# Optimization experiments

Hardware: AMD Instinct MI355X
Metric: run time of the kernel (lower is better)

## Reference

```python
import jax, jax.numpy as jnp
import numpy as np

NUM_HEADS = 32
HEAD_DIM = 64
ROPE_THETA = 10000.0


def _rope_cos_sin(position_ids, head_dim, theta):
    # inv_freq: [head_dim/2]
    half = head_dim // 2
    inv_freq = 1.0 / (theta ** (jnp.arange(0, half, dtype=jnp.float32) * 2.0 / head_dim))
    angles = position_ids.astype(jnp.float32)[..., None] * inv_freq  # [B,S,half]
    return jnp.cos(angles), jnp.sin(angles)


def _apply_rope(x, cos, sin):
    # x: [B,S,H,hd]; cos/sin: [B,S,half] -> broadcast over heads (rotate-half, Llama style)
    half = x.shape[-1] // 2
    x1, x2 = x[..., :half], x[..., half:]
    c = cos[:, :, None, :]
    s = sin[:, :, None, :]
    return jnp.concatenate([x1 * c - x2 * s, x2 * c + x1 * s], axis=-1)


def setup_inputs() -> dict:
    key = jax.random.key(0)
    ks = jax.random.split(key, 8)
    B, S, D = 2, 2048, 2048
    hidden_states = jax.random.normal(ks[0], (B, S, D), dtype=jnp.float32)
    # causal additive mask (is_causal=False in IpexSDP; mask carries causality)
    causal = jnp.tril(jnp.ones((S, S), dtype=jnp.bool_))
    attention_mask = jnp.where(causal, 0.0, -1e9).astype(jnp.float32)[None, None, :, :]
    attention_mask = jnp.broadcast_to(attention_mask, (B, 1, S, S))
    position_ids = jnp.broadcast_to(jnp.arange(S, dtype=jnp.int64)[None, :], (B, S))
    scale = 0.02
    qkv_w = jax.random.normal(ks[1], (3, D, D), dtype=jnp.float32) * scale
    qkv_b = jax.random.normal(ks[2], (3, D), dtype=jnp.float32) * scale
    o_w = jax.random.normal(ks[3], (D, D), dtype=jnp.float32) * scale
    o_b = jax.random.normal(ks[4], (D,), dtype=jnp.float32) * scale
    residual = jax.random.normal(ks[5], (B, S, D), dtype=jnp.float32)
    return {
        'hidden_states': hidden_states,
        'attention_mask': attention_mask,
        'position_ids': position_ids,
        'qkv_w': qkv_w,
        'qkv_b': qkv_b,
        'o_w': o_w,
        'o_b': o_b,
        'residual': residual,
    }


def reference(hidden_states, attention_mask, position_ids, qkv_w, qkv_b, o_w, o_b, residual):
    B, S, D = hidden_states.shape
    H, hd = NUM_HEADS, HEAD_DIM
    # fused QKV projection (weights stored transposed: x @ W), matching mm_qkv_out
    qkv = jnp.einsum('bsd,tde->tbse', hidden_states, qkv_w) + qkv_b[:, None, None, :]
    q = qkv[0].reshape(B, S, H, hd)
    k = qkv[1].reshape(B, S, H, hd)
    v = qkv[2].reshape(B, S, H, hd)
    cos, sin = _rope_cos_sin(position_ids, hd, ROPE_THETA)
    q = _apply_rope(q, cos, sin)
    k = _apply_rope(k, cos, sin)
    scale = 1.0 / jnp.sqrt(jnp.asarray(hd, dtype=hidden_states.dtype))
    # [B,H,S,S]
    scores = jnp.einsum('bqhd,bkhd->bhqk', q, k) * scale + attention_mask
    probs = jax.nn.softmax(scores, axis=-1)
    attn = jnp.einsum('bhqk,bkhd->bqhd', probs, v).reshape(B, S, D)
    # o-proj fused with bias + residual add (matmul_add_add)
    out = attn @ o_w + o_b + residual
    return out
```

## Files before the change

kernel.cpp:

```cpp
#include <hip/hip_runtime.h>
#include <stdint.h>
#include <stdio.h>

#define D_MODEL 2048
#define SEQ     2048
#define NHEADS  32
#define HDIM    64
#define BATCH   2
#define BH      (BATCH * NHEADS)
#define GK      2048

typedef unsigned short u16;
typedef unsigned int   u32;
typedef __attribute__((ext_vector_type(8))) short short8;
typedef __attribute__((ext_vector_type(4))) short s16x4;
typedef __attribute__((ext_vector_type(4))) float f32x4;
typedef __attribute__((ext_vector_type(4))) u32   u32x4;
typedef __attribute__((ext_vector_type(2))) u32   u32x2;

__device__ __forceinline__ float bf2f(u16 x) {
  union { u32 u; float f; } c; c.u = ((u32)x) << 16; return c.f;
}
__device__ __forceinline__ u16 f2bf(float f) {
  union { float f; u32 u; } c; c.f = f;
  u32 u = c.u;
  return (u16)((u + 0x7FFFu + ((u >> 16) & 1u)) >> 16);
}
__device__ __forceinline__ u32 fbits(float f) {
  union { float f; u32 u; } c; c.f = f; return c.u;
}

typedef const __attribute__((address_space(1))) u32* gas_t;
typedef __attribute__((address_space(3))) u32* las_t;
__device__ __forceinline__ void gll16(const void* g, void* l) {
  __builtin_amdgcn_global_load_lds((gas_t)g, (las_t)l, 16, 0, 0);
}

__device__ __forceinline__ void swiz_mn(int pid, int nx, int& mtile, int& ntile) {
  int chunk = 8 * nx;
  int grp = pid / chunk, loc = pid - grp * chunk;
  mtile = grp * 8 + (loc & 7);
  ntile = loc >> 3;
}

__global__ __launch_bounds__(256) void cvt_k(const float* __restrict__ in,
                                             u16* __restrict__ out) {
  int id = blockIdx.x * 256 + threadIdx.x;
  f32x4 v = *(const f32x4*)&in[(size_t)id * 4];
  alignas(8) u16 o[4];
#pragma unroll
  for (int j = 0; j < 4; j++) o[j] = f2bf(v[j]);
  *(u32x2*)&out[(size_t)id * 4] = *(const u32x2*)o;
}

__global__ __launch_bounds__(256) void transpose_cvt_k(const float* __restrict__ qkv_w,
                                                       const float* __restrict__ o_w,
                                                       u16* __restrict__ outT) {
  __shared__ u16 tile[64][72];
  const int z = blockIdx.z;
  const float* inz = (z < 3) ? qkv_w + (size_t)z * D_MODEL * D_MODEL : o_w;
  u16* outz = outT + (size_t)z * D_MODEL * D_MODEL;
  const int r0 = blockIdx.y * 64, c0 = blockIdx.x * 64;
  const int t = threadIdx.x;
  const int lrow = t >> 4, lcol4 = (t & 15) * 4;
#pragma unroll
  for (int i = 0; i < 4; i++) {
    int r = lrow + i * 16;
    f32x4 v = *(const f32x4*)&inz[(size_t)(r0 + r) * D_MODEL + (c0 + lcol4)];
#pragma unroll
    for (int j = 0; j < 4; j++) tile[r][lcol4 + j] = f2bf(v[j]);
  }
  __syncthreads();
  const int row = t >> 3, col8 = (t & 7) * 8;
#pragma unroll
  for (int i = 0; i < 2; i++) {
    int r = row + i * 32;
    alignas(16) u16 vals[8];
#pragma unroll
    for (int j = 0; j < 8; j++) vals[j] = tile[col8 + j][r];
    *(u32x4*)&outz[(size_t)(c0 + r) * D_MODEL + (r0 + col8)] = *(const u32x4*)vals;
  }
}

__device__ __forceinline__ void gemm128(const u16* __restrict__ A, const u16* __restrict__ BT,
                                        int m0, int n0, u16* As, u16* Bs, f32x4 acc[4][4]) {
  const int t = threadIdx.x;
  const int lane = t & 63, w = t >> 6;
  const int quad = lane >> 4, l16 = lane & 15;
  const int wr = w >> 1, wc = w & 1;
  const int ldr = lane >> 2, ldc = (lane & 3) * 8;
#pragma unroll
  for (int mt = 0; mt < 4; mt++)
#pragma unroll
    for (int nt = 0; nt < 4; nt++)
#pragma unroll
      for (int i = 0; i < 4; i++) acc[mt][nt][i] = 0.0f;

  for (int k0 = 0; k0 < GK; k0 += 32) {
    __syncthreads();
#pragma unroll
    for (int i = 0; i < 2; i++) {
      int rbase = w * 32 + i * 16;
      gll16(&A[(size_t)(m0 + rbase + ldr) * GK + k0 + ldc], &As[rbase * 32]);
      gll16(&BT[(size_t)(n0 + rbase + ldr) * GK + k0 + ldc], &Bs[rbase * 32]);
    }
    __syncthreads();
    short8 af[4], bf[4];
#pragma unroll
    for (int mt = 0; mt < 4; mt++)
      af[mt] = *(const short8*)&As[(wr * 64 + mt * 16 + l16) * 32 + quad * 8];
#pragma unroll
    for (int nt = 0; nt < 4; nt++)
      bf[nt] = *(const short8*)&Bs[(wc * 64 + nt * 16 + l16) * 32 + quad * 8];
#pragma unroll
    for (int mt = 0; mt < 4; mt++)
#pragma unroll
      for (int nt = 0; nt < 4; nt++)
        acc[mt][nt] = __builtin_amdgcn_mfma_f32_16x16x32_bf16(af[mt], bf[nt], acc[mt][nt], 0, 0, 0);
  }
}

__global__ __launch_bounds__(256) void qkv_gemm_k(const u16* __restrict__ A, const u16* __restrict__ BT,
                                                  const float* __restrict__ bias,
                                                  u16* __restrict__ Qb, u16* __restrict__ Kb,
                                                  u16* __restrict__ Vbt) {
  __shared__ u16 As[128 * 32], Bs[128 * 32];
  f32x4 acc[4][4];
  int mtile, ntile;
  swiz_mn(blockIdx.x, 48, mtile, ntile);
  const int m0 = mtile * 128, n0 = ntile * 128;
  gemm128(A, BT, m0, n0, As, Bs, acc);
  const int t = threadIdx.x, lane = t & 63, quad = lane >> 4, l16 = lane & 15;
  const int w = t >> 6, wr = w >> 1, wc = w & 1;
  const int tsel = n0 >> 11;

  if (tsel < 2) {
    u16* dst = tsel ? Kb : Qb;
#pragma unroll
    for (int p = 0; p < 2; p++) {
      int nlo = n0 + wc * 64 + p * 16 + l16;
      float blo = bias[nlo], bhi = bias[nlo + 32];
      int j = p * 16 + l16;
      float inv = __expf((float)j * -0.28782313662425572f);
      int h = (nlo & 2047) >> 6;
#pragma unroll
      for (int mt = 0; mt < 4; mt++) {
#pragma unroll
        for (int r = 0; r < 4; r++) {
          int m = m0 + wr * 64 + mt * 16 + quad * 4 + r;
          int b = m >> 11, s = m & (SEQ - 1);
          float sn, cs;
          __sincosf((float)s * inv, &sn, &cs);
          float x1 = acc[mt][p][r] + blo;
          float x2 = acc[mt][p + 2][r] + bhi;
          size_t base = ((size_t)((b * NHEADS + h) * SEQ + s)) * HDIM;
          dst[base + j]      = f2bf(x1 * cs - x2 * sn);
          dst[base + j + 32] = f2bf(x2 * cs + x1 * sn);
        }
      }
    }
  } else {
#pragma unroll
    for (int nt = 0; nt < 4; nt++) {
      int n = n0 + wc * 64 + nt * 16 + l16;
      float bv = bias[n];
      int e = n & 2047, h = e >> 6, d = e & 63;
#pragma unroll
      for (int mt = 0; mt < 4; mt++) {
        int m0r = m0 + wr * 64 + mt * 16 + quad * 4;
        int b = m0r >> 11, s0 = m0r & (SEQ - 1);
        alignas(8) u16 o4[4];
#pragma unroll
        for (int r = 0; r < 4; r++) o4[r] = f2bf(acc[mt][nt][r] + bv);
        *(u32x2*)&Vbt[((size_t)((b * NHEADS + h) * HDIM + d)) * SEQ + s0] = *(const u32x2*)o4;
      }
    }
  }
}

__global__ __launch_bounds__(256) void oproj_gemm_k(const u16* __restrict__ A, const u16* __restrict__ BT,
                                                    const float* __restrict__ bias,
                                                    const float* __restrict__ resid,
                                                    float* __restrict__ out) {
  __shared__ u16 As[128 * 32], Bs[128 * 32];
  f32x4 acc[4][4];
  int mtile, ntile;
  swiz_mn(blockIdx.x, 16, mtile, ntile);
  const int m0 = mtile * 128, n0 = ntile * 128;
  gemm128(A, BT, m0, n0, As, Bs, acc);
  const int t = threadIdx.x, lane = t & 63, quad = lane >> 4, l16 = lane & 15;
  const int w = t >> 6, wr = w >> 1, wc = w & 1;
#pragma unroll
  for (int nt = 0; nt < 4; nt++) {
    int n = n0 + wc * 64 + nt * 16 + l16;
    float bv = bias[n];
#pragma unroll
    for (int mt = 0; mt < 4; mt++) {
#pragma unroll
      for (int r = 0; r < 4; r++) {
        int m = m0 + wr * 64 + mt * 16 + quad * 4 + r;
        size_t oi = (size_t)m * D_MODEL + n;
        out[oi] = acc[mt][nt][r] + bv + resid[oi];
      }
    }
  }
}

__global__ __launch_bounds__(256, 4) void attn_k(const u16* __restrict__ Qb,
                                                 const u16* __restrict__ Kb,
                                                 const u16* __restrict__ Vbt,
                                                 u16* __restrict__ attn) {
  __shared__ u16 smem[128 * 72];
  u16* Ks = smem;
  u16* Vt = smem + 64 * 72;
  const int blk = blockIdx.x;
  const int qt16 = blk & 15, bh = blk >> 4;
  const int b = bh >> 5, h = bh & 31;
  const int t = threadIdx.x, w = t >> 6, lane = t & 63, quad = lane >> 4, l16 = lane & 15;
  const int qbase = qt16 * 128, qw = qbase + w * 32;
  const size_t bho = (size_t)bh * SEQ * HDIM;
  const size_t vbo = (size_t)bh * HDIM * SEQ;

  short8 qf[2][2];
#pragma unroll
  for (int qt = 0; qt < 2; qt++)
#pragma unroll
    for (int kd = 0; kd < 2; kd++) {
      short8 v = *(const short8*)&Qb[bho + (size_t)(qw + qt * 16 + l16) * HDIM + kd * 32 + quad * 8];
#pragma unroll
      for (int i = 0; i < 8; i++) {
        float f = bf2f((u16)v[i]) * 0.125f;
        v[i] = (short)f2bf(f);
      }
      qf[qt][kd] = v;
    }

  f32x4 Oacc[4][2];
  float mrow[2] = {-1e30f, -1e30f}, lrow[2] = {0.0f, 0.0f};
#pragma unroll
  for (int dt = 0; dt < 4; dt++)
#pragma unroll
    for (int qt = 0; qt < 2; qt++)
#pragma unroll
      for (int i = 0; i < 4; i++) Oacc[dt][qt][i] = 0.0f;

  const int srow = t >> 3, scol = (t & 7) * 8;
  const int kend = qbase + 128;

  for (int key0 = 0; key0 < kend; key0 += 64) {
    __syncthreads();
    *(u32x4*)&Ks[srow * 72 + scol] =
        *(const u32x4*)&Kb[bho + (size_t)(key0 + srow) * HDIM + scol];
    *(u32x4*)&Ks[(srow + 32) * 72 + scol] =
        *(const u32x4*)&Kb[bho + (size_t)(key0 + srow + 32) * HDIM + scol];
    *(u32x4*)&Vt[srow * 72 + scol] =
        *(const u32x4*)&Vbt[vbo + (size_t)srow * SEQ + key0 + scol];
    *(u32x4*)&Vt[(srow + 32) * 72 + scol] =
        *(const u32x4*)&Vbt[vbo + (size_t)(srow + 32) * SEQ + key0 + scol];
    __syncthreads();

    if (key0 <= qw + 31) {
      f32x4 sacc[4][2];
#pragma unroll
      for (int kt = 0; kt < 4; kt++) {
        short8 kf0 = *(const short8*)&Ks[(kt * 16 + l16) * 72 + quad * 8];
        short8 kf1 = *(const short8*)&Ks[(kt * 16 + l16) * 72 + 32 + quad * 8];
#pragma unroll
        for (int qt = 0; qt < 2; qt++) {
#pragma unroll
          for (int i = 0; i < 4; i++) sacc[kt][qt][i] = 0.0f;
          sacc[kt][qt] = __builtin_amdgcn_mfma_f32_16x16x32_bf16(kf0, qf[qt][0], sacc[kt][qt], 0, 0, 0);
          sacc[kt][qt] = __builtin_amdgcn_mfma_f32_16x16x32_bf16(kf1, qf[qt][1], sacc[kt][qt], 0, 0, 0);
        }
      }
      if (key0 + 63 > qw) {
#pragma unroll
        for (int qt = 0; qt < 2; qt++) {
          int qrow = qw + qt * 16 + l16;
#pragma unroll
          for (int kt = 0; kt < 4; kt++)
#pragma unroll
            for (int r = 0; r < 4; r++)
              if (key0 + kt * 16 + quad * 4 + r > qrow) sacc[kt][qt][r] = -1e30f;
        }
      }
      float alpha[2];
#pragma unroll
      for (int qt = 0; qt < 2; qt++) {
        float mx = sacc[0][qt][0];
#pragma unroll
        for (int kt = 0; kt < 4; kt++)
#pragma unroll
          for (int r = 0; r < 4; r++) mx = fmaxf(mx, sacc[kt][qt][r]);
        mx = fmaxf(mx, __shfl_xor(mx, 16));
        mx = fmaxf(mx, __shfl_xor(mx, 32));
        float mnew = fmaxf(mrow[qt], mx);
        alpha[qt] = __expf(mrow[qt] - mnew);
        mrow[qt] = mnew;
        float rsum = 0.0f;
#pragma unroll
        for (int kt = 0; kt < 4; kt++)
#pragma unroll
          for (int r = 0; r < 4; r++) {
            float pv = __expf(sacc[kt][qt][r] - mnew);
            sacc[kt][qt][r] = pv;
            rsum += pv;
          }
        rsum += __shfl_xor(rsum, 16);
        rsum += __shfl_xor(rsum, 32);
        lrow[qt] = lrow[qt] * alpha[qt] + rsum;
      }
#pragma unroll
      for (int dt = 0; dt < 4; dt++)
#pragma unroll
        for (int qt = 0; qt < 2; qt++)
#pragma unroll
          for (int r = 0; r < 4; r++) Oacc[dt][qt][r] *= alpha[qt];

      s16x4 pk[4][2];
#pragma unroll
      for (int kt = 0; kt < 4; kt++)
#pragma unroll
        for (int qt = 0; qt < 2; qt++) {
          u32 a0 = fbits(sacc[kt][qt][0]) + 0x8000u;
          u32 a1 = fbits(sacc[kt][qt][1]) + 0x8000u;
          u32 a2 = fbits(sacc[kt][qt][2]) + 0x8000u;
          u32 a3 = fbits(sacc[kt][qt][3]) + 0x8000u;
          union { u32 u[2]; s16x4 s; } pc;
          pc.u[0] = __builtin_amdgcn_perm(a1, a0, 0x07060302u);
          pc.u[1] = __builtin_amdgcn_perm(a3, a2, 0x07060302u);
          pk[kt][qt] = pc.s;
        }
#pragma unroll
      for (int kt = 0; kt < 4; kt++) {
        s16x4 vf[4];
#pragma unroll
        for (int dt = 0; dt < 4; dt++)
          vf[dt] = *(const s16x4*)&Vt[(dt * 16 + l16) * 72 + kt * 16 + quad * 4];
#pragma unroll
        for (int dt = 0; dt < 4; dt++)
#pragma unroll
          for (int qt = 0; qt < 2; qt++)
            Oacc[dt][qt] = __builtin_amdgcn_mfma_f32_16x16x16bf16_1k(vf[dt], pk[kt][qt], Oacc[dt][qt], 0, 0, 0);
      }
    }
  }

  __syncthreads();
  float invl[2] = {1.0f / lrow[0], 1.0f / lrow[1]};
#pragma unroll
  for (int dt = 0; dt < 4; dt++)
#pragma unroll
    for (int qt = 0; qt < 2; qt++)
#pragma unroll
      for (int r = 0; r < 4; r++)
        smem[(w * 32 + qt * 16 + l16) * 72 + dt * 16 + quad * 4 + r] =
            f2bf(Oacc[dt][qt][r] * invl[qt]);
  __syncthreads();
#pragma unroll
  for (int i = 0; i < 4; i++) {
    int chunk = t + i * 256;
    int row = chunk >> 3, g = chunk & 7;
    *(u32x4*)&attn[((size_t)(b * SEQ + qbase + row)) * D_MODEL + h * 64 + g * 8] =
        *(const u32x4*)&smem[row * 72 + g * 8];
  }
}

extern "C" void kernel_launch(void* const* d_in, const int* in_sizes, int n_in,
                              void* d_out, int out_size, void* d_ws, size_t ws_size,
                              hipStream_t stream) {
  (void)in_sizes; (void)n_in; (void)out_size;
  const float* hidden = (const float*)d_in[0];
  const float* qkv_w = (const float*)d_in[3];
  const float* qkv_b = (const float*)d_in[4];
  const float* o_w   = (const float*)d_in[5];
  const float* o_b   = (const float*)d_in[6];
  const float* resid = (const float*)d_in[7];
  float* out = (float*)d_out;

  u16* ws = (u16*)d_ws;
  size_t off = 0;
  u16* hidb  = ws + off; off += (size_t)BATCH * SEQ * D_MODEL;
  u16* qkvT  = ws + off; off += (size_t)3 * D_MODEL * D_MODEL;
  u16* owT   = ws + off; off += (size_t)D_MODEL * D_MODEL;
  u16* Qb    = ws + off; off += (size_t)BH * SEQ * HDIM;
  u16* Kb    = ws + off; off += (size_t)BH * SEQ * HDIM;
  u16* Vbt   = ws + off; off += (size_t)BH * SEQ * HDIM;
  u16* attnb = ws + off; off += (size_t)BATCH * SEQ * D_MODEL;
  if (ws_size < off * sizeof(u16)) {
    fprintf(stderr, "kernel_launch: workspace too small: need %zu bytes, have %zu\n",
            off * sizeof(u16), ws_size);
    return;
  }
  (void)owT;

  cvt_k<<<(BATCH * SEQ * D_MODEL) / (4 * 256), 256, 0, stream>>>(hidden, hidb);
  transpose_cvt_k<<<dim3(32, 32, 4), 256, 0, stream>>>(qkv_w, o_w, qkvT);
  qkv_gemm_k<<<48 * 32, 256, 0, stream>>>(hidb, qkvT, qkv_b, Qb, Kb, Vbt);
  attn_k<<<BH * (SEQ / 128), 256, 0, stream>>>(Qb, Kb, Vbt, attnb);
  oproj_gemm_k<<<16 * 32, 256, 0, stream>>>(attnb, owT, o_b, resid, out);
}
```

Before: 485.4 us.

## Pair causal query tiles per block and prefetch K/V through registers

Each attention block now handles two query tiles, pi and 15-pi, so every block does the same amount of causal work and shares the K/V tiles loaded into LDS between them. The next K/V tile is loaded into registers while the current tile is computed, which overlaps global loads with MFMA work. Key sub-tiles that lie entirely above the diagonal are skipped. The grid is halved and launch bounds relaxed to 2 waves, which raises register use and lowers occupancy in exchange.

```diff
diff --git a/kernel.cpp b/kernel.cpp
--- a/kernel.cpp
+++ b/kernel.cpp
@@ -206,7 +206,7 @@
   }
 }
 
-__global__ __launch_bounds__(256, 4) void attn_k(const u16* __restrict__ Qb,
+__global__ __launch_bounds__(256, 2) void attn_k(const u16* __restrict__ Qb,
                                                  const u16* __restrict__ Kb,
                                                  const u16* __restrict__ Vbt,
                                                  u16* __restrict__ attn) {
@@ -214,155 +214,193 @@
   u16* Ks = smem;
   u16* Vt = smem + 64 * 72;
   const int blk = blockIdx.x;
-  const int qt16 = blk & 15, bh = blk >> 4;
+  const int bh = blk & 63, pi = blk >> 6;
   const int b = bh >> 5, h = bh & 31;
   const int t = threadIdx.x, w = t >> 6, lane = t & 63, quad = lane >> 4, l16 = lane & 15;
-  const int qbase = qt16 * 128, qw = qbase + w * 32;
+  const int qbT[2] = { pi * 128, (15 - pi) * 128 };
+  const int qwT[2] = { qbT[0] + w * 32, qbT[1] + w * 32 };
   const size_t bho = (size_t)bh * SEQ * HDIM;
   const size_t vbo = (size_t)bh * HDIM * SEQ;
-
-  short8 qf[2][2];
-#pragma unroll
-  for (int qt = 0; qt < 2; qt++)
-#pragma unroll
-    for (int kd = 0; kd < 2; kd++) {
-      short8 v = *(const short8*)&Qb[bho + (size_t)(qw + qt * 16 + l16) * HDIM + kd * 32 + quad * 8];
-#pragma unroll
-      for (int i = 0; i < 8; i++) {
-        float f = bf2f((u16)v[i]) * 0.125f;
-        v[i] = (short)f2bf(f);
-      }
-      qf[qt][kd] = v;
-    }
-
-  f32x4 Oacc[4][2];
-  float mrow[2] = {-1e30f, -1e30f}, lrow[2] = {0.0f, 0.0f};
-#pragma unroll
-  for (int dt = 0; dt < 4; dt++)
+  const int kend = qbT[1] + 128;
+
+  short8 qf[2][2][2];
+#pragma unroll
+  for (int Ti = 0; Ti < 2; Ti++)
 #pragma unroll
     for (int qt = 0; qt < 2; qt++)
 #pragma unroll
-      for (int i = 0; i < 4; i++) Oacc[dt][qt][i] = 0.0f;
-
-  const int srow = t >> 3, scol = (t & 7) * 8;
-  const int kend = qbase + 128;
+      for (int kd = 0; kd < 2; kd++) {
+        short8 v = *(const short8*)&Qb[bho + (size_t)(qwT[Ti] + qt * 16 + l16) * HDIM + kd * 32 + quad * 8];
+#pragma unroll
+        for (int i = 0; i < 8; i++) {
+          float f = bf2f((u16)v[i]) * 0.125f;
+          v[i] = (short)f2bf(f);
+        }
+        qf[Ti][qt][kd] = v;
+      }
+
+  f32x4 Oacc[2][4][2];
+  float mrow[2][2] = {{-1e30f, -1e30f}, {-1e30f, -1e30f}};
+  float lrow[2][2] = {{0.0f, 0.0f}, {0.0f, 0.0f}};
+#pragma unroll
+  for (int Ti = 0; Ti < 2; Ti++)
+#pragma unroll
+    for (int dt = 0; dt < 4; dt++)
+#pragma unroll
+      for (int qt = 0; qt < 2; qt++)
+#pragma unroll
+        for (int i = 0; i < 4; i++) Oacc[Ti][dt][qt][i] = 0.0f;
+
+  const int srow = t >> 3, sc8 = (t & 7) * 8;
+  u32x4 kreg[2], vreg[2];
+
+#pragma unroll
+  for (int j = 0; j < 2; j++) {
+    kreg[j] = *(const u32x4*)&Kb[bho + (size_t)(srow + j * 32) * HDIM + sc8];
+    vreg[j] = *(const u32x4*)&Vbt[vbo + (size_t)(srow + j * 32) * SEQ + sc8];
+  }
+#pragma unroll
+  for (int j = 0; j < 2; j++) {
+    *(u32x4*)&Ks[(srow + j * 32) * 72 + sc8] = kreg[j];
+    *(u32x4*)&Vt[(srow + j * 32) * 72 + sc8] = vreg[j];
+  }
+  __syncthreads();
 
   for (int key0 = 0; key0 < kend; key0 += 64) {
+    const int nxt = key0 + 64;
+    if (nxt < kend) {
+#pragma unroll
+      for (int j = 0; j < 2; j++) {
+        kreg[j] = *(const u32x4*)&Kb[bho + (size_t)(nxt + srow + j * 32) * HDIM + sc8];
+        vreg[j] = *(const u32x4*)&Vbt[vbo + (size_t)(srow + j * 32) * SEQ + nxt + sc8];
+      }
+    }
+#pragma unroll
+    for (int Ti = 0; Ti < 2; Ti++) {
+      const int qw = qwT[Ti];
+      if (key0 <= qw + 31) {
+        const int lim = qw + 31 - key0;
+        int nkt = (lim >> 4) + 1; if (nkt > 4) nkt = 4;
+        f32x4 sacc[4][2];
+#pragma unroll
+        for (int kt = 0; kt < 4; kt++) {
+          if (kt < nkt) {
+            short8 kf0 = *(const short8*)&Ks[(kt * 16 + l16) * 72 + quad * 8];
+            short8 kf1 = *(const short8*)&Ks[(kt * 16 + l16) * 72 + 32 + quad * 8];
+#pragma unroll
+            for (int qt = 0; qt < 2; qt++) {
+              f32x4 z = {0.0f, 0.0f, 0.0f, 0.0f};
+              z = __builtin_amdgcn_mfma_f32_16x16x32_bf16(kf0, qf[Ti][qt][0], z, 0, 0, 0);
+              z = __builtin_amdgcn_mfma_f32_16x16x32_bf16(kf1, qf[Ti][qt][1], z, 0, 0, 0);
+              sacc[kt][qt] = z;
+            }
+          }
+        }
+        if (key0 + 63 > qw) {
+#pragma unroll
+          for (int qt = 0; qt < 2; qt++) {
+            int qrow = qw + qt * 16 + l16;
+#pragma unroll
+            for (int kt = 0; kt < 4; kt++)
+              if (kt < nkt)
+#pragma unroll
+                for (int r = 0; r < 4; r++)
+                  if (key0 + kt * 16 + quad * 4 + r > qrow) sacc[kt][qt][r] = -1e30f;
+          }
+        }
+        float alpha[2];
+#pragma unroll
+        for (int qt = 0; qt < 2; qt++) {
+          float mx = -1e30f;
+#pragma unroll
+          for (int kt = 0; kt < 4; kt++)
+            if (kt < nkt)
+#pragma unroll
+              for (int r = 0; r < 4; r++) mx = fmaxf(mx, sacc[kt][qt][r]);
+          mx = fmaxf(mx, __shfl_xor(mx, 16));
+          mx = fmaxf(mx, __shfl_xor(mx, 32));
+          float mnew = fmaxf(mrow[Ti][qt], mx);
+          alpha[qt] = __expf(mrow[Ti][qt] - mnew);
+          mrow[Ti][qt] = mnew;
+          float rsum = 0.0f;
+#pragma unroll
+          for (int kt = 0; kt < 4; kt++)
+            if (kt < nkt)
+#pragma unroll
+              for (int r = 0; r < 4; r++) {
+                float pv = __expf(sacc[kt][qt][r] - mnew);
+                sacc[kt][qt][r] = pv;
+                rsum += pv;
+              }
+          rsum += __shfl_xor(rsum, 16);
+          rsum += __shfl_xor(rsum, 32);
+          lrow[Ti][qt] = lrow[Ti][qt] * alpha[qt] + rsum;
+        }
+#pragma unroll
+        for (int dt = 0; dt < 4; dt++)
+#pragma unroll
+          for (int qt = 0; qt < 2; qt++)
+#pragma unroll
+            for (int r = 0; r < 4; r++) Oacc[Ti][dt][qt][r] *= alpha[qt];
+#pragma unroll
+        for (int kt = 0; kt < 4; kt++) {
+          if (kt < nkt) {
+            s16x4 pk[2];
+#pragma unroll
+            for (int qt = 0; qt < 2; qt++) {
+              u32 a0 = fbits(sacc[kt][qt][0]) + 0x8000u;
+              u32 a1 = fbits(sacc[kt][qt][1]) + 0x8000u;
+              u32 a2 = fbits(sacc[kt][qt][2]) + 0x8000u;
+              u32 a3 = fbits(sacc[kt][qt][3]) + 0x8000u;
+              union { u32 u[2]; s16x4 s; } pc;
+              pc.u[0] = __builtin_amdgcn_perm(a1, a0, 0x07060302u);
+              pc.u[1] = __builtin_amdgcn_perm(a3, a2, 0x07060302u);
+              pk[qt] = pc.s;
+            }
+            s16x4 vf[4];
+#pragma unroll
+            for (int dt = 0; dt < 4; dt++)
+              vf[dt] = *(const s16x4*)&Vt[(dt * 16 + l16) * 72 + kt * 16 + quad * 4];
+#pragma unroll
+            for (int dt = 0; dt < 4; dt++)
+#pragma unroll
+              for (int qt = 0; qt < 2; qt++)
+                Oacc[Ti][dt][qt] = __builtin_amdgcn_mfma_f32_16x16x16bf16_1k(vf[dt], pk[qt], Oacc[Ti][dt][qt], 0, 0, 0);
+          }
+        }
+      }
+    }
     __syncthreads();
-    *(u32x4*)&Ks[srow * 72 + scol] =
-        *(const u32x4*)&Kb[bho + (size_t)(key0 + srow) * HDIM + scol];
-    *(u32x4*)&Ks[(srow + 32) * 72 + scol] =
-        *(const u32x4*)&Kb[bho + (size_t)(key0 + srow + 32) * HDIM + scol];
-    *(u32x4*)&Vt[srow * 72 + scol] =
-        *(const u32x4*)&Vbt[vbo + (size_t)srow * SEQ + key0 + scol];
-    *(u32x4*)&Vt[(srow + 32) * 72 + scol] =
-        *(const u32x4*)&Vbt[vbo + (size_t)(srow + 32) * SEQ + key0 + scol];
+    if (nxt < kend) {
+#pragma unroll
+      for (int j = 0; j < 2; j++) {
+        *(u32x4*)&Ks[(srow + j * 32) * 72 + sc8] = kreg[j];
+        *(u32x4*)&Vt[(srow + j * 32) * 72 + sc8] = vreg[j];
+      }
+      __syncthreads();
+    }
+  }
+
+#pragma unroll
+  for (int Ti = 0; Ti < 2; Ti++) {
+    float invl[2] = {1.0f / lrow[Ti][0], 1.0f / lrow[Ti][1]};
+#pragma unroll
+    for (int dt = 0; dt < 4; dt++)
+#pragma unroll
+      for (int qt = 0; qt < 2; qt++)
+#pragma unroll
+        for (int r = 0; r < 4; r++)
+          smem[(w * 32 + qt * 16 + l16) * 72 + dt * 16 + quad * 4 + r] =
+              f2bf(Oacc[Ti][dt][qt][r] * invl[qt]);
     __syncthreads();
-
-    if (key0 <= qw + 31) {
-      f32x4 sacc[4][2];
-#pragma unroll
-      for (int kt = 0; kt < 4; kt++) {
-        short8 kf0 = *(const short8*)&Ks[(kt * 16 + l16) * 72 + quad * 8];
-        short8 kf1 = *(const short8*)&Ks[(kt * 16 + l16) * 72 + 32 + quad * 8];
-#pragma unroll
-        for (int qt = 0; qt < 2; qt++) {
-#pragma unroll
-          for (int i = 0; i < 4; i++) sacc[kt][qt][i] = 0.0f;
-          sacc[kt][qt] = __builtin_amdgcn_mfma_f32_16x16x32_bf16(kf0, qf[qt][0], sacc[kt][qt], 0, 0, 0);
-          sacc[kt][qt] = __builtin_amdgcn_mfma_f32_16x16x32_bf16(kf1, qf[qt][1], sacc[kt][qt], 0, 0, 0);
-        }
-      }
-      if (key0 + 63 > qw) {
-#pragma unroll
-        for (int qt = 0; qt < 2; qt++) {
-          int qrow = qw + qt * 16 + l16;
-#pragma unroll
-          for (int kt = 0; kt < 4; kt++)
-#pragma unroll
-            for (int r = 0; r < 4; r++)
-              if (key0 + kt * 16 + quad * 4 + r > qrow) sacc[kt][qt][r] = -1e30f;
-        }
-      }
-      float alpha[2];
-#pragma unroll
-      for (int qt = 0; qt < 2; qt++) {
-        float mx = sacc[0][qt][0];
-#pragma unroll
-        for (int kt = 0; kt < 4; kt++)
-#pragma unroll
-          for (int r = 0; r < 4; r++) mx = fmaxf(mx, sacc[kt][qt][r]);
-        mx = fmaxf(mx, __shfl_xor(mx, 16));
-        mx = fmaxf(mx, __shfl_xor(mx, 32));
-        float mnew = fmaxf(mrow[qt], mx);
-        alpha[qt] = __expf(mrow[qt] - mnew);
-        mrow[qt] = mnew;
-        float rsum = 0.0f;
-#pragma unroll
-        for (int kt = 0; kt < 4; kt++)
-#pragma unroll
-          for (int r = 0; r < 4; r++) {
-            float pv = __expf(sacc[kt][qt][r] - mnew);
-            sacc[kt][qt][r] = pv;
-            rsum += pv;
-          }
-        rsum += __shfl_xor(rsum, 16);
-        rsum += __shfl_xor(rsum, 32);
-        lrow[qt] = lrow[qt] * alpha[qt] + rsum;
-      }
-#pragma unroll
-      for (int dt = 0; dt < 4; dt++)
-#pragma unroll
-        for (int qt = 0; qt < 2; qt++)
-#pragma unroll
-          for (int r = 0; r < 4; r++) Oacc[dt][qt][r] *= alpha[qt];
-
-      s16x4 pk[4][2];
-#pragma unroll
-      for (int kt = 0; kt < 4; kt++)
-#pragma unroll
-        for (int qt = 0; qt < 2; qt++) {
-          u32 a0 = fbits(sacc[kt][qt][0]) + 0x8000u;
-          u32 a1 = fbits(sacc[kt][qt][1]) + 0x8000u;
-          u32 a2 = fbits(sacc[kt][qt][2]) + 0x8000u;
-          u32 a3 = fbits(sacc[kt][qt][3]) + 0x8000u;
-          union { u32 u[2]; s16x4 s; } pc;
-          pc.u[0] = __builtin_amdgcn_perm(a1, a0, 0x07060302u);
-          pc.u[1] = __builtin_amdgcn_perm(a3, a2, 0x07060302u);
-          pk[kt][qt] = pc.s;
-        }
-#pragma unroll
-      for (int kt = 0; kt < 4; kt++) {
-        s16x4 vf[4];
-#pragma unroll
-        for (int dt = 0; dt < 4; dt++)
-          vf[dt] = *(const s16x4*)&Vt[(dt * 16 + l16) * 72 + kt * 16 + quad * 4];
-#pragma unroll
-        for (int dt = 0; dt < 4; dt++)
-#pragma unroll
-          for (int qt = 0; qt < 2; qt++)
-            Oacc[dt][qt] = __builtin_amdgcn_mfma_f32_16x16x16bf16_1k(vf[dt], pk[kt][qt], Oacc[dt][qt], 0, 0, 0);
-      }
-    }
-  }
-
-  __syncthreads();
-  float invl[2] = {1.0f / lrow[0], 1.0f / lrow[1]};
-#pragma unroll
-  for (int dt = 0; dt < 4; dt++)
-#pragma unroll
-    for (int qt = 0; qt < 2; qt++)
-#pragma unroll
-      for (int r = 0; r < 4; r++)
-        smem[(w * 32 + qt * 16 + l16) * 72 + dt * 16 + quad * 4 + r] =
-            f2bf(Oacc[dt][qt][r] * invl[qt]);
-  __syncthreads();
-#pragma unroll
-  for (int i = 0; i < 4; i++) {
-    int chunk = t + i * 256;
-    int row = chunk >> 3, g = chunk & 7;
-    *(u32x4*)&attn[((size_t)(b * SEQ + qbase + row)) * D_MODEL + h * 64 + g * 8] =
-        *(const u32x4*)&smem[row * 72 + g * 8];
+#pragma unroll
+    for (int ii = 0; ii < 4; ii++) {
+      int chunk = t + ii * 256;
+      int row = chunk >> 3, g = chunk & 7;
+      *(u32x4*)&attn[((size_t)(b * SEQ + qbT[Ti] + row)) * D_MODEL + h * 64 + g * 8] =
+          *(const u32x4*)&smem[row * 72 + g * 8];
+    }
+    __syncthreads();
   }
 }
 
@@ -397,6 +435,6 @@
   cvt_k<<<(BATCH * SEQ * D_MODEL) / (4 * 256), 256, 0, stream>>>(hidden, hidb);
   transpose_cvt_k<<<dim3(32, 32, 4), 256, 0, stream>>>(qkv_w, o_w, qkvT);
   qkv_gemm_k<<<48 * 32, 256, 0, stream>>>(hidb, qkvT, qkv_b, Qb, Kb, Vbt);
-  attn_k<<<BH * (SEQ / 128), 256, 0, stream>>>(Qb, Kb, Vbt, attnb);
+  attn_k<<<BH * 8, 256, 0, stream>>>(Qb, Kb, Vbt, attnb);
   oproj_gemm_k<<<16 * 32, 256, 0, stream>>>(attnb, owT, o_b, resid, out);
 }
```

Measured after the change: 443.1 us. -8.7%, faster.
